# Kernel tuning notes

Hardware: AMD Instinct MI355X
Metric: run time of the kernel (lower is better)

The kernel has to match this reference:

```python
import jax, jax.numpy as jnp
import numpy as np

B, C, H, W = 4, 256, 64, 64
D_STATE, D_CONV, EXPAND = 16, 4, 2
D_INNER = EXPAND * C          # 512
DT_RANK = (C + 15) // 16      # 16 (math.ceil(d_model/16), mamba_ssm default)


def setup_inputs() -> dict:
    key = jax.random.key(0)
    ks = jax.random.split(key, 16)
    s = lambda k, shp, sc=0.02: (jax.random.normal(k, shp, dtype=jnp.float32) * sc)
    inp = {
        "spatial_feat": jax.random.normal(ks[0], (B, C, H, W), dtype=jnp.float32),
        "freq_feat":    jax.random.normal(ks[1], (B, C, H, W), dtype=jnp.float32),
        # fusion proj: Linear(2C -> C)
        "W_proj": s(ks[2], (C, 2 * C)),
        "b_proj": jnp.zeros((C,), jnp.float32),
        # Mamba params (mamba_ssm defaults: bias=False for in/out proj, conv_bias=True)
        "W_in":   s(ks[3], (2 * D_INNER, C)),
        "conv_w": s(ks[4], (D_INNER, 1, D_CONV), 0.1),
        "conv_b": jnp.zeros((D_INNER,), jnp.float32),
        "W_x":    s(ks[5], (DT_RANK + 2 * D_STATE, D_INNER)),
        "W_dt":   s(ks[6], (D_INNER, DT_RANK), 0.1),
        "b_dt":   s(ks[7], (D_INNER,), 0.5),
        "A_log":  jnp.log(jnp.tile(jnp.arange(1, D_STATE + 1, dtype=jnp.float32), (D_INNER, 1))),
        "D":      jnp.ones((D_INNER,), jnp.float32),
        "W_out":  s(ks[8], (C, D_INNER)),
        # LayerNorm
        "ln_gamma": jnp.ones((C,), jnp.float32),
        "ln_beta":  jnp.zeros((C,), jnp.float32),
    }
    return inp


def _mamba(x, W_in, conv_w, conv_b, W_x, W_dt, b_dt, A_log, Dp, W_out):
    # x: [B, L, C]
    Bb, L, _ = x.shape
    xz = jnp.einsum("blc,ec->ble", x, W_in)              # [B,L,2*d_inner]
    u, z = jnp.split(xz, 2, axis=-1)                      # each [B,L,d_inner]
    # causal depthwise conv1d along L
    u_c = jnp.transpose(u, (0, 2, 1))                     # [B,d_inner,L]
    u_c = jax.lax.conv_general_dilated(
        u_c, conv_w, window_strides=(1,), padding=[(D_CONV - 1, 0)],
        dimension_numbers=("NCH", "OIH", "NCH"), feature_group_count=D_INNER)
    u_c = u_c + conv_b[None, :, None]
    u = jax.nn.silu(jnp.transpose(u_c, (0, 2, 1)))        # [B,L,d_inner]
    # input-dependent dt, B, C
    dbc = jnp.einsum("bld,rd->blr", u, W_x)               # [B,L,dt_rank+2*d_state]
    dt = dbc[..., :DT_RANK]
    Bm = dbc[..., DT_RANK:DT_RANK + D_STATE]              # [B,L,d_state]
    Cm = dbc[..., DT_RANK + D_STATE:]                     # [B,L,d_state]
    delta = jax.nn.softplus(jnp.einsum("blr,dr->bld", dt, W_dt) + b_dt)  # [B,L,d_inner]
    A = -jnp.exp(A_log)                                   # [d_inner,d_state]

    def step(h, t):
        delta_t, B_t, C_t, u_t = t                        # [B,di],[B,ds],[B,ds],[B,di]
        dA = jnp.exp(delta_t[..., None] * A)              # [B,di,ds]
        h = h * dA + (delta_t * u_t)[..., None] * B_t[:, None, :]
        y = jnp.einsum("bds,bs->bd", h, C_t)
        return h, y

    tm = lambda a: jnp.swapaxes(a, 0, 1)                  # [B,L,..] -> [L,B,..]
    h0 = jnp.zeros((Bb, D_INNER, D_STATE), x.dtype)
    _, ys = jax.lax.scan(step, h0, (tm(delta), tm(Bm), tm(Cm), tm(u)))
    y = jnp.swapaxes(ys, 0, 1)                            # [B,L,d_inner]
    y = y + u * Dp
    y = y * jax.nn.silu(z)
    return jnp.einsum("bld,cd->blc", y, W_out)            # [B,L,C]


def reference(spatial_feat, freq_feat, W_proj, b_proj, W_in, conv_w, conv_b,
              W_x, W_dt, b_dt, A_log, D, W_out, ln_gamma, ln_beta):
    Bb, Cc, Hh, Ww = spatial_feat.shape
    L = Hh * Ww
    xs = jnp.transpose(spatial_feat.reshape(Bb, Cc, L), (0, 2, 1))  # [B,L,C]
    xf = jnp.transpose(freq_feat.reshape(Bb, Cc, L), (0, 2, 1))
    x_cat = jnp.concatenate([xs, xf], axis=-1)                       # [B,L,2C]
    x_proj = jnp.einsum("ble,ce->blc", x_cat, W_proj) + b_proj       # [B,L,C]
    x_mixed = _mamba(x_proj, W_in, conv_w, conv_b, W_x, W_dt, b_dt, A_log, D, W_out)
    mu = jnp.mean(x_mixed, axis=-1, keepdims=True)
    var = jnp.var(x_mixed, axis=-1, keepdims=True)
    x_out = (x_mixed - mu) * jax.lax.rsqrt(var + 1e-5) * ln_gamma + ln_beta
    return jnp.transpose(x_out, (0, 2, 1)).reshape(Bb, Cc, Hh, Ww)
```

## Files before the change

kernel.cpp:

```cpp
#include <hip/hip_runtime.h>
#include <hip/hip_fp16.h>
#include <math.h>

#define L 4096
#define CDIM 256
#define DIN 512
#define DSTATE 16
#define DTR 16
#define BATCH 4

using f32x4  = __attribute__((ext_vector_type(4))) float;
using f16x8  = __attribute__((ext_vector_type(8))) _Float16;

__device__ __forceinline__ float silu_f(float x) { return x / (1.f + __expf(-x)); }
__device__ __forceinline__ float softplus_fast(float x) {
    return (x > 20.f) ? x : __logf(1.f + __expf(x));
}
__device__ __forceinline__ unsigned pk2h(float a, float b) {
    __half2 h = __floats2half2_rn(a, b);
    return *reinterpret_cast<unsigned*>(&h);
}

#define LDK 40

enum { HEPI_XP = 0, HEPI_UZ = 1, HEPI_F32 = 2, HEPI_D34 = 3 };
template<int EPI, bool A_F32KM, int NT>
__global__ __launch_bounds__(256)
void hgemm(const float* __restrict__ Af0, const float* __restrict__ Af1,
           const __half* __restrict__ Ah_g, const __half* __restrict__ Bh_g,
           const float* __restrict__ bias,
           float* __restrict__ O0, __half* __restrict__ Oh0, __half* __restrict__ Oh1,
           float* __restrict__ Ob, float* __restrict__ Oc,
           int M, int N, int K, int kSplit, long strideAb, int nBlk)
{
    constexpr int BM = 64, MT = 2;
    constexpr int BN = 2 * NT * 16;
    constexpr int BSEG = BN / 64;
    __shared__ __align__(16) _Float16 Ah[2][BM][LDK];
    __shared__ __align__(16) _Float16 Bh[2][BN][LDK];
    const int mBlk = M / BM;
    const int bid = blockIdx.x;
    const int r = bid & 7, q = bid >> 3;
    const int ni = q % nBlk;
    const int mg = (q / nBlk) * 8 + r;
    const int b = mg / mBlk, m_idx = mg - b * mBlk;
    const int n0 = ni * BN, m0 = m_idx * BM;
    const int tid  = threadIdx.x;
    const int lane = tid & 63;
    const int w    = tid >> 6;
    const int wr   = w >> 1, wc = w & 1;
    const int lrow = lane & 15;
    const int loct = lane >> 4;

    f32x4 acc[MT][NT];
    #pragma unroll
    for (int i = 0; i < MT; ++i)
        #pragma unroll
        for (int j = 0; j < NT; ++j)
            acc[i][j] = (f32x4){0.f, 0.f, 0.f, 0.f};

    const int sOct = tid & 3, sRow = tid >> 2;
    float va[8];
    uint4 pa, pb[BSEG];

    auto loadA = [&](int kk) {
        if (A_F32KM) {
            int m = tid & 63, ks = tid >> 6;
            #pragma unroll
            for (int j = 0; j < 8; ++j) {
                int kg = kk + ks * 8 + j;
                const float* Ap; int kl;
                if (kg < kSplit) { Ap = Af0; kl = kg; } else { Ap = Af1; kl = kg - kSplit; }
                va[j] = Ap[(long)b * strideAb + (long)kl * M + m0 + m];
            }
        } else {
            pa = *(const uint4*)(Ah_g + (long)b * strideAb +
                                 (long)(m0 + sRow) * K + kk + sOct * 8);
        }
    };
    auto loadB = [&](int kk) {
        #pragma unroll
        for (int p = 0; p < BSEG; ++p) {
            int ng = n0 + sRow + p * 64;
            if (EPI == HEPI_D34 && ng >= N)
                pb[p] = make_uint4(0, 0, 0, 0);
            else
                pb[p] = *(const uint4*)(Bh_g + (long)ng * K + kk + sOct * 8);
        }
    };
    auto storeAB = [&](int buf) {
        if (A_F32KM) {
            int m = tid & 63, ks = tid >> 6;
            uint4 h;
            h.x = pk2h(va[0], va[1]);
            h.y = pk2h(va[2], va[3]);
            h.z = pk2h(va[4], va[5]);
            h.w = pk2h(va[6], va[7]);
            *(uint4*)&Ah[buf][m][ks * 8] = h;
        } else {
            *(uint4*)&Ah[buf][sRow][sOct * 8] = pa;
        }
        #pragma unroll
        for (int p = 0; p < BSEG; ++p)
            *(uint4*)&Bh[buf][sRow + p * 64][sOct * 8] = pb[p];
    };

    loadA(0); loadB(0);
    storeAB(0);
    __syncthreads();
    int cur = 0;
    for (int kk = 0; kk < K; kk += 32) {
        const bool more = (kk + 32 < K);
        if (more) { loadA(kk + 32); loadB(kk + 32); }
        f16x8 bh[NT];
        #pragma unroll
        for (int nt = 0; nt < NT; ++nt)
            bh[nt] = *(const f16x8*)&Bh[cur][wc*NT*16 + nt*16 + lrow][loct*8];
        #pragma unroll
        for (int mt = 0; mt < MT; ++mt) {
            f16x8 ah = *(const f16x8*)&Ah[cur][wr*MT*16 + mt*16 + lrow][loct*8];
            #pragma unroll
            for (int nt = 0; nt < NT; ++nt)
                acc[mt][nt] = __builtin_amdgcn_mfma_f32_16x16x32_f16(ah, bh[nt], acc[mt][nt], 0, 0, 0);
        }
        if (more) {
            storeAB(cur ^ 1);
            __syncthreads();
            cur ^= 1;
        }
    }
    #pragma unroll
    for (int mt = 0; mt < MT; ++mt) {
        #pragma unroll
        for (int r4 = 0; r4 < 4; ++r4) {
            int m = m0 + wr*MT*16 + mt * 16 + loct * 4 + r4;
            long rowb = (long)b * M + m;
            #pragma unroll
            for (int nt = 0; nt < NT; ++nt) {
                int n = n0 + wc*NT*16 + nt * 16 + lrow;
                float v = acc[mt][nt][r4];
                if (EPI == HEPI_XP) {
                    Oh0[rowb * N + n] = __float2half(v + bias[n]);
                } else if (EPI == HEPI_UZ) {
                    if (n < DIN) Oh0[rowb * DIN + n] = __float2half(v);
                    else         Oh1[rowb * DIN + (n - DIN)] = __float2half(v);
                } else if (EPI == HEPI_D34) {
                    if (n < DTR)           O0[rowb * DTR + n] = v;
                    else if (n < 2 * DTR)  Ob[rowb * 16 + (n - DTR)] = v;
                    else if (n < 48)       Oc[rowb * 16 + (n - 32)] = v;
                } else {
                    O0[rowb * N + n] = v;
                }
            }
        }
    }
}

#define SZ_WP  131072
#define SZ_WIN 262144
#define SZ_WO  131072
#define SZ_WC  24576
__global__ __launch_bounds__(256)
void pack_all(const float* __restrict__ Wp, const float* __restrict__ Win,
              const float* __restrict__ Wout, const float* __restrict__ Wx,
              __half* __restrict__ wph, __half* __restrict__ winh,
              __half* __restrict__ woh, __half* __restrict__ wch)
{
    int i = blockIdx.x * 256 + threadIdx.x;
    if (i < SZ_WP) { wph[i] = __float2half(Wp[i]); return; }
    i -= SZ_WP;
    if (i < SZ_WIN) { winh[i] = __float2half(Win[i]); return; }
    i -= SZ_WIN;
    if (i < SZ_WO) { woh[i] = __float2half(Wout[i]); return; }
    i -= SZ_WO;
    if (i < SZ_WC) wch[i] = __float2half(Wx[i]);
}

__global__ __launch_bounds__(256)
void conv_silu_kernel(const __half* __restrict__ u_pre, const float* __restrict__ cw,
                      const float* __restrict__ cb, __half* __restrict__ u)
{
    long idx = (long)blockIdx.x * blockDim.x + threadIdx.x;
    int d = (int)(idx % DIN);
    long bl = idx / DIN;
    int l = (int)(bl % L);
    long brow = bl - l;
    float v = cb[d];
    #pragma unroll
    for (int j = 0; j < 4; ++j) {
        int li = l - 3 + j;
        if (li >= 0) v += __half2float(u_pre[(brow + li) * DIN + d]) * cw[d * 4 + j];
    }
    u[idx] = __float2half(silu_f(v));
}

#define NC 128
#define LC (L / NC)

__global__ __launch_bounds__(256)
void scan_phase1(const float* __restrict__ dtA, const __half* __restrict__ u,
                 const float* __restrict__ Bm, const float* __restrict__ A_log,
                 const float* __restrict__ Wdt, const float* __restrict__ bdt,
                 float* __restrict__ Asum, float* __restrict__ Xsum)
{
    __shared__ float sB[LC][DSTATE];
    __shared__ float sDt[LC][DTR];
    const int gd = blockIdx.x & 1;
    const int c  = (blockIdx.x >> 1) & (NC - 1);
    const int b  = blockIdx.x >> 8;
    const int d  = gd * 256 + threadIdx.x;
    const int t0 = c * LC;
    float Arow[DSTATE];
    #pragma unroll
    for (int q = 0; q < 4; ++q) {
        float4 v = *(const float4*)&A_log[d * DSTATE + q * 4];
        Arow[q * 4 + 0] = -__expf(v.x);
        Arow[q * 4 + 1] = -__expf(v.y);
        Arow[q * 4 + 2] = -__expf(v.z);
        Arow[q * 4 + 3] = -__expf(v.w);
    }
    float Wrow[DTR];
    #pragma unroll
    for (int q = 0; q < 4; ++q) {
        float4 v = *(const float4*)&Wdt[d * DTR + q * 4];
        Wrow[q * 4 + 0] = v.x; Wrow[q * 4 + 1] = v.y;
        Wrow[q * 4 + 2] = v.z; Wrow[q * 4 + 3] = v.w;
    }
    const float bd = bdt[d];
    for (int i = threadIdx.x; i < LC * DSTATE; i += 256) {
        long row = (long)b * L + t0 + (i >> 4);
        sB[i >> 4][i & 15]  = Bm[row * DSTATE + (i & 15)];
        sDt[i >> 4][i & 15] = dtA[row * DTR + (i & 15)];
    }
    __syncthreads();
    float P[DSTATE], X[DSTATE];
    #pragma unroll
    for (int s = 0; s < DSTATE; ++s) { P[s] = 1.f; X[s] = 0.f; }
    for (int t = 0; t < LC; ++t) {
        long gidx = ((long)b * L + t0 + t) * DIN + d;
        float dp = bd;
        #pragma unroll
        for (int rr = 0; rr < DTR; ++rr) dp += sDt[t][rr] * Wrow[rr];
        float dlt = softplus_fast(dp);
        float du  = dlt * __half2float(u[gidx]);
        #pragma unroll
        for (int s = 0; s < DSTATE; ++s) {
            float a = __expf(dlt * Arow[s]);
            P[s] *= a;
            X[s] = a * X[s] + du * sB[t][s];
        }
    }
    long o = (((long)b * NC + c) * DIN + d) * DSTATE;
    #pragma unroll
    for (int q = 0; q < 4; ++q) {
        *(float4*)&Asum[o + q * 4] = make_float4(P[q*4], P[q*4+1], P[q*4+2], P[q*4+3]);
        *(float4*)&Xsum[o + q * 4] = make_float4(X[q*4], X[q*4+1], X[q*4+2], X[q*4+3]);
    }
}

__global__ __launch_bounds__(256)
void scan_phase2(const float* __restrict__ Asum, float* __restrict__ Xsum)
{
    int lane = blockIdx.x * 256 + threadIdx.x;
    int b = lane / (DIN * DSTATE);
    int rem = lane % (DIN * DSTATE);
    float h = 0.f;
    for (int c = 0; c < NC; ++c) {
        long idx = ((long)b * NC + c) * (DIN * DSTATE) + rem;
        float A = Asum[idx], X = Xsum[idx];
        Xsum[idx] = h;
        h = A * h + X;
    }
}

__global__ __launch_bounds__(256)
void scan_phase3(const float* __restrict__ dtA, const __half* __restrict__ u,
                 const float* __restrict__ Bm, const float* __restrict__ Cm,
                 const __half* __restrict__ z, const float* __restrict__ A_log,
                 const float* __restrict__ Wdt, const float* __restrict__ bdt,
                 const float* __restrict__ Dp, const float* __restrict__ Hinit,
                 __half* __restrict__ y2h)
{
    __shared__ float sB[LC][DSTATE], sC[LC][DSTATE];
    __shared__ float sDt[LC][DTR];
    const int gd = blockIdx.x & 1;
    const int c  = (blockIdx.x >> 1) & (NC - 1);
    const int b  = blockIdx.x >> 8;
    const int d  = gd * 256 + threadIdx.x;
    const int t0 = c * LC;
    float Arow[DSTATE];
    #pragma unroll
    for (int q = 0; q < 4; ++q) {
        float4 v = *(const float4*)&A_log[d * DSTATE + q * 4];
        Arow[q * 4 + 0] = -__expf(v.x);
        Arow[q * 4 + 1] = -__expf(v.y);
        Arow[q * 4 + 2] = -__expf(v.z);
        Arow[q * 4 + 3] = -__expf(v.w);
    }
    float Wrow[DTR];
    #pragma unroll
    for (int q = 0; q < 4; ++q) {
        float4 v = *(const float4*)&Wdt[d * DTR + q * 4];
        Wrow[q * 4 + 0] = v.x; Wrow[q * 4 + 1] = v.y;
        Wrow[q * 4 + 2] = v.z; Wrow[q * 4 + 3] = v.w;
    }
    const float bd = bdt[d];
    for (int i = threadIdx.x; i < LC * DSTATE; i += 256) {
        long row = (long)b * L + t0 + (i >> 4);
        long gidx = row * DSTATE + (i & 15);
        sB[i >> 4][i & 15]  = Bm[gidx];
        sC[i >> 4][i & 15]  = Cm[gidx];
        sDt[i >> 4][i & 15] = dtA[row * DTR + (i & 15)];
    }
    float h[DSTATE];
    {
        long o = (((long)b * NC + c) * DIN + d) * DSTATE;
        #pragma unroll
        for (int q = 0; q < 4; ++q) {
            float4 v = *(const float4*)&Hinit[o + q * 4];
            h[q * 4 + 0] = v.x; h[q * 4 + 1] = v.y;
            h[q * 4 + 2] = v.z; h[q * 4 + 3] = v.w;
        }
    }
    const float Dval = Dp[d];
    __syncthreads();
    for (int t = 0; t < LC; ++t) {
        long gidx = ((long)b * L + t0 + t) * DIN + d;
        float dp = bd;
        #pragma unroll
        for (int rr = 0; rr < DTR; ++rr) dp += sDt[t][rr] * Wrow[rr];
        float dlt = softplus_fast(dp);
        float uu  = __half2float(u[gidx]);
        float zz  = __half2float(z[gidx]);
        float du  = dlt * uu;
        float y = 0.f;
        #pragma unroll
        for (int s = 0; s < DSTATE; ++s) {
            float a = __expf(dlt * Arow[s]);
            h[s] = h[s] * a + du * sB[t][s];
            y += h[s] * sC[t][s];
        }
        y2h[gidx] = __float2half((y + uu * Dval) * silu_f(zz));
    }
}

__global__ __launch_bounds__(256)
void ln_kernel(const float* __restrict__ X, const float* __restrict__ gamma,
               const float* __restrict__ beta, float* __restrict__ out)
{
    __shared__ float tile[32][257];
    __shared__ float sMu[32], sRs[32];
    const int l0 = blockIdx.x * 32;
    const int b  = blockIdx.y;
    const int tid = threadIdx.x;
    for (int i = tid; i < 32 * 256; i += 256) {
        int l = i >> 8, c = i & 255;
        tile[l][c] = X[((long)b * L + l0 + l) * CDIM + c];
    }
    __syncthreads();
    {
        int l = tid >> 3, sub = tid & 7;
        float s1 = 0.f, s2 = 0.f;
        for (int c = sub * 32; c < sub * 32 + 32; ++c) {
            float v = tile[l][c];
            s1 += v; s2 += v * v;
        }
        s1 += __shfl_xor(s1, 1); s2 += __shfl_xor(s2, 1);
        s1 += __shfl_xor(s1, 2); s2 += __shfl_xor(s2, 2);
        s1 += __shfl_xor(s1, 4); s2 += __shfl_xor(s2, 4);
        if (sub == 0) {
            float mu = s1 * (1.f / 256.f);
            float var = s2 * (1.f / 256.f) - mu * mu;
            sMu[l] = mu;
            sRs[l] = rsqrtf(var + 1e-5f);
        }
    }
    __syncthreads();
    for (int i = tid; i < 32 * 256; i += 256) {
        int ll = i & 31, c = i >> 5;
        float v = (tile[ll][c] - sMu[ll]) * sRs[ll] * gamma[c] + beta[c];
        out[((long)b * CDIM + c) * L + l0 + ll] = v;
    }
}

extern "C" void kernel_launch(void* const* d_in, const int* in_sizes, int n_in,
                              void* d_out, int out_size, void* d_ws, size_t ws_size,
                              hipStream_t stream)
{
    const float* sp   = (const float*)d_in[0];
    const float* fq   = (const float*)d_in[1];
    const float* Wp   = (const float*)d_in[2];
    const float* bp   = (const float*)d_in[3];
    const float* Win  = (const float*)d_in[4];
    const float* cw   = (const float*)d_in[5];
    const float* cb   = (const float*)d_in[6];
    const float* Wx   = (const float*)d_in[7];
    const float* Wdt  = (const float*)d_in[8];
    const float* bdt  = (const float*)d_in[9];
    const float* Alog = (const float*)d_in[10];
    const float* Dp   = (const float*)d_in[11];
    const float* Wout = (const float*)d_in[12];
    const float* gam  = (const float*)d_in[13];
    const float* bet  = (const float*)d_in[14];
    float* out = (float*)d_out;
    float* ws  = (float*)d_ws;

    const size_t NLD = (size_t)BATCH * L * DIN;
    const size_t NLC = (size_t)BATCH * L * CDIM;

    size_t off = 0;
    __half* u16   = (__half*)(ws + off); off += NLD / 2;
    __half* u16c  = (__half*)(ws + off); off += NLD / 2;
    __half* z16   = (__half*)(ws + off); off += NLD / 2;
    __half* y16   = (__half*)(ws + off); off += NLD / 2;
    __half* xp16  = (__half*)(ws + off); off += NLC / 2;
    float*  xmix  = ws + off; off += NLC;
    float*  dtA   = ws + off; off += (size_t)BATCH * L * DTR;
    __half* wph   = (__half*)(ws + off); off += SZ_WP / 2;
    __half* winh  = (__half*)(ws + off); off += SZ_WIN / 2;
    __half* woh   = (__half*)(ws + off); off += SZ_WO / 2;
    __half* wch   = (__half*)(ws + off); off += SZ_WC / 2;
    float*  Bmb   = ws + off; off += (size_t)BATCH * L * DSTATE;
    float*  Cmb   = ws + off; off += (size_t)BATCH * L * DSTATE;
    float*  Asum  = ws + off; off += (size_t)BATCH * NC * DIN * DSTATE;
    float*  Xsum  = ws + off; off += (size_t)BATCH * NC * DIN * DSTATE;

    dim3 blk(256);
    pack_all<<<dim3((SZ_WP + SZ_WIN + SZ_WO + SZ_WC) / 256), blk, 0, stream>>>(
        Wp, Win, Wout, Wx, wph, winh, woh, wch);

    hgemm<HEPI_XP, true, 2><<<dim3(BATCH * (L/64) * 4), blk, 0, stream>>>(
        sp, fq, nullptr, wph, bp, nullptr, xp16, nullptr, nullptr, nullptr,
        L, CDIM, 2 * CDIM, CDIM, (long)CDIM * L, 4);
    hgemm<HEPI_UZ, false, 4><<<dim3(BATCH * (L/64) * 8), blk, 0, stream>>>(
        nullptr, nullptr, xp16, winh, nullptr, nullptr, u16, z16, nullptr, nullptr,
        L, 2 * DIN, CDIM, 1 << 30, (long)L * CDIM, 8);
    conv_silu_kernel<<<dim3((int)(NLD / 256)), blk, 0, stream>>>(u16, cw, cb, u16c);
    hgemm<HEPI_D34, false, 2><<<dim3(BATCH * (L/64) * 1), blk, 0, stream>>>(
        nullptr, nullptr, u16c, wch, nullptr, dtA, nullptr, nullptr, Bmb, Cmb,
        L, 48, DIN, 1 << 30, (long)L * DIN, 1);

    scan_phase1<<<dim3(BATCH * NC * 2), blk, 0, stream>>>(
        dtA, u16c, Bmb, Alog, Wdt, bdt, Asum, Xsum);
    scan_phase2<<<dim3(BATCH * DIN * DSTATE / 256), blk, 0, stream>>>(Asum, Xsum);
    scan_phase3<<<dim3(BATCH * NC * 2), blk, 0, stream>>>(
        dtA, u16c, Bmb, Cmb, z16, Alog, Wdt, bdt, Dp, Xsum, y16);

    hgemm<HEPI_F32, false, 2><<<dim3(BATCH * (L/64) * 4), blk, 0, stream>>>(
        nullptr, nullptr, y16, woh, nullptr, xmix, nullptr, nullptr, nullptr, nullptr,
        L, CDIM, DIN, 1 << 30, (long)L * DIN, 4);
    ln_kernel<<<dim3(L / 32, BATCH), blk, 0, stream>>>(xmix, gam, bet, out);
}
```

Before: 344.1 us.

## Stage scan inputs in shared memory, use exp2, interleave chunk summaries, prefetch phase2

The scan phases now preload each chunk's u and z halves into shared memory with vectorized 16-byte loads, and load B, C and dt rows as float4. The per-step exp uses a hardware exp2 builtin with A prescaled by log2(e). Phase 1 writes the chunk decay and state interleaved into one AX buffer, and phase 2 prefetches eight chunks ahead and writes its prefix states to a separate Hout buffer. The dt dot product is split into four partial sums, and phase 3 accumulates y in four partial sums to shorten dependency chains. This aims to cut global-load latency and transcendental cost in the scan, at the price of more shared memory per block and possibly lower occupancy.

```diff
diff --git a/kernel.cpp b/kernel.cpp
--- a/kernel.cpp
+++ b/kernel.cpp
@@ -12,7 +12,17 @@
 using f32x4  = __attribute__((ext_vector_type(4))) float;
 using f16x8  = __attribute__((ext_vector_type(8))) _Float16;
 
-__device__ __forceinline__ float silu_f(float x) { return x / (1.f + __expf(-x)); }
+#define LOG2E 1.44269504088896f
+
+#if __has_builtin(__builtin_amdgcn_exp2f)
+#define EXP2(x) __builtin_amdgcn_exp2f(x)
+#else
+#define EXP2(x) __expf((x) * 0.69314718056f)
+#endif
+
+__device__ __forceinline__ float silu_f(float x) {
+    return __fdividef(x, 1.f + __expf(-x));
+}
 __device__ __forceinline__ float softplus_fast(float x) {
     return (x > 20.f) ? x : __logf(1.f + __expf(x));
 }
@@ -201,75 +211,103 @@
 void scan_phase1(const float* __restrict__ dtA, const __half* __restrict__ u,
                  const float* __restrict__ Bm, const float* __restrict__ A_log,
                  const float* __restrict__ Wdt, const float* __restrict__ bdt,
-                 float* __restrict__ Asum, float* __restrict__ Xsum)
+                 float* __restrict__ AX)
 {
     __shared__ float sB[LC][DSTATE];
     __shared__ float sDt[LC][DTR];
+    __shared__ __half sU[LC][256];
     const int gd = blockIdx.x & 1;
     const int c  = (blockIdx.x >> 1) & (NC - 1);
     const int b  = blockIdx.x >> 8;
-    const int d  = gd * 256 + threadIdx.x;
+    const int tid = threadIdx.x;
+    const int d  = gd * 256 + tid;
     const int t0 = c * LC;
     float Arow[DSTATE];
     #pragma unroll
     for (int q = 0; q < 4; ++q) {
         float4 v = *(const float4*)&A_log[d * DSTATE + q * 4];
-        Arow[q * 4 + 0] = -__expf(v.x);
-        Arow[q * 4 + 1] = -__expf(v.y);
-        Arow[q * 4 + 2] = -__expf(v.z);
-        Arow[q * 4 + 3] = -__expf(v.w);
-    }
-    float Wrow[DTR];
-    #pragma unroll
-    for (int q = 0; q < 4; ++q) {
-        float4 v = *(const float4*)&Wdt[d * DTR + q * 4];
-        Wrow[q * 4 + 0] = v.x; Wrow[q * 4 + 1] = v.y;
-        Wrow[q * 4 + 2] = v.z; Wrow[q * 4 + 3] = v.w;
-    }
+        Arow[q * 4 + 0] = -__expf(v.x) * LOG2E;
+        Arow[q * 4 + 1] = -__expf(v.y) * LOG2E;
+        Arow[q * 4 + 2] = -__expf(v.z) * LOG2E;
+        Arow[q * 4 + 3] = -__expf(v.w) * LOG2E;
+    }
+    const float4 W0 = *(const float4*)&Wdt[d * DTR + 0];
+    const float4 W1 = *(const float4*)&Wdt[d * DTR + 4];
+    const float4 W2 = *(const float4*)&Wdt[d * DTR + 8];
+    const float4 W3 = *(const float4*)&Wdt[d * DTR + 12];
     const float bd = bdt[d];
-    for (int i = threadIdx.x; i < LC * DSTATE; i += 256) {
-        long row = (long)b * L + t0 + (i >> 4);
-        sB[i >> 4][i & 15]  = Bm[row * DSTATE + (i & 15)];
-        sDt[i >> 4][i & 15] = dtA[row * DTR + (i & 15)];
+    {
+        const __half* ub = u + ((long)b * L + t0) * DIN + gd * 256;
+        #pragma unroll
+        for (int j = 0; j < 4; ++j) {
+            int i = tid + j * 256;
+            int t = i >> 5, col = (i & 31) * 8;
+            *(float4*)&sU[t][col] = *(const float4*)&ub[(long)t * DIN + col];
+        }
+        if (tid < 128) {
+            const float* Bb = Bm  + ((long)b * L + t0) * DSTATE;
+            const float* Db = dtA + ((long)b * L + t0) * DTR;
+            *(float4*)&((float*)sB)[tid * 4]  = *(const float4*)&Bb[tid * 4];
+            *(float4*)&((float*)sDt)[tid * 4] = *(const float4*)&Db[tid * 4];
+        }
     }
     __syncthreads();
     float P[DSTATE], X[DSTATE];
     #pragma unroll
     for (int s = 0; s < DSTATE; ++s) { P[s] = 1.f; X[s] = 0.f; }
+    #pragma unroll 2
     for (int t = 0; t < LC; ++t) {
-        long gidx = ((long)b * L + t0 + t) * DIN + d;
-        float dp = bd;
-        #pragma unroll
-        for (int rr = 0; rr < DTR; ++rr) dp += sDt[t][rr] * Wrow[rr];
-        float dlt = softplus_fast(dp);
-        float du  = dlt * __half2float(u[gidx]);
+        float4 q0 = *(const float4*)&sDt[t][0];
+        float4 q1 = *(const float4*)&sDt[t][4];
+        float4 q2 = *(const float4*)&sDt[t][8];
+        float4 q3 = *(const float4*)&sDt[t][12];
+        float dp0 = fmaf(q0.x, W0.x, fmaf(q0.y, W0.y, fmaf(q0.z, W0.z, q0.w * W0.w)));
+        float dp1 = fmaf(q1.x, W1.x, fmaf(q1.y, W1.y, fmaf(q1.z, W1.z, q1.w * W1.w)));
+        float dp2 = fmaf(q2.x, W2.x, fmaf(q2.y, W2.y, fmaf(q2.z, W2.z, q2.w * W2.w)));
+        float dp3 = fmaf(q3.x, W3.x, fmaf(q3.y, W3.y, fmaf(q3.z, W3.z, q3.w * W3.w)));
+        float dlt = softplus_fast(((dp0 + dp1) + (dp2 + dp3)) + bd);
+        float du  = dlt * __half2float(sU[t][tid]);
+        float Brow[DSTATE];
+        *(float4*)&Brow[0]  = *(const float4*)&sB[t][0];
+        *(float4*)&Brow[4]  = *(const float4*)&sB[t][4];
+        *(float4*)&Brow[8]  = *(const float4*)&sB[t][8];
+        *(float4*)&Brow[12] = *(const float4*)&sB[t][12];
         #pragma unroll
         for (int s = 0; s < DSTATE; ++s) {
-            float a = __expf(dlt * Arow[s]);
+            float a = EXP2(dlt * Arow[s]);
             P[s] *= a;
-            X[s] = a * X[s] + du * sB[t][s];
-        }
-    }
-    long o = (((long)b * NC + c) * DIN + d) * DSTATE;
-    #pragma unroll
-    for (int q = 0; q < 4; ++q) {
-        *(float4*)&Asum[o + q * 4] = make_float4(P[q*4], P[q*4+1], P[q*4+2], P[q*4+3]);
-        *(float4*)&Xsum[o + q * 4] = make_float4(X[q*4], X[q*4+1], X[q*4+2], X[q*4+3]);
-    }
-}
-
-__global__ __launch_bounds__(256)
-void scan_phase2(const float* __restrict__ Asum, float* __restrict__ Xsum)
+            X[s] = fmaf(a, X[s], du * Brow[s]);
+        }
+    }
+    long o2 = ((((long)b * NC + c) * DIN + d) * DSTATE) * 2;
+    #pragma unroll
+    for (int q = 0; q < 8; ++q)
+        *(float4*)&AX[o2 + q * 4] =
+            make_float4(P[2*q], X[2*q], P[2*q+1], X[2*q+1]);
+}
+
+__global__ __launch_bounds__(256)
+void scan_phase2(const float* __restrict__ AX, float* __restrict__ Hout)
 {
     int lane = blockIdx.x * 256 + threadIdx.x;
-    int b = lane / (DIN * DSTATE);
-    int rem = lane % (DIN * DSTATE);
+    int b = lane >> 13;
+    int rem = lane & 8191;
+    const long cs = (long)DIN * DSTATE;
+    const long base = (long)b * NC * cs + rem;
     float h = 0.f;
-    for (int c = 0; c < NC; ++c) {
-        long idx = ((long)b * NC + c) * (DIN * DSTATE) + rem;
-        float A = Asum[idx], X = Xsum[idx];
-        Xsum[idx] = h;
-        h = A * h + X;
+    float2 c0, c1, c2, c3, n0, n1, n2, n3;
+    auto ld = [&](int c) -> float2 {
+        return *(const float2*)&AX[2 * (base + (long)c * cs)];
+    };
+    c0 = ld(0); c1 = ld(1); c2 = ld(2); c3 = ld(3);
+    n0 = ld(4); n1 = ld(5); n2 = ld(6); n3 = ld(7);
+    for (int c = 0; c < NC; c += 4) {
+        Hout[base + (long)(c+0) * cs] = h; h = fmaf(c0.x, h, c0.y);
+        Hout[base + (long)(c+1) * cs] = h; h = fmaf(c1.x, h, c1.y);
+        Hout[base + (long)(c+2) * cs] = h; h = fmaf(c2.x, h, c2.y);
+        Hout[base + (long)(c+3) * cs] = h; h = fmaf(c3.x, h, c3.y);
+        c0 = n0; c1 = n1; c2 = n2; c3 = n3;
+        if (c + 8 < NC) { n0 = ld(c+8); n1 = ld(c+9); n2 = ld(c+10); n3 = ld(c+11); }
     }
 }
 
@@ -283,34 +321,46 @@
 {
     __shared__ float sB[LC][DSTATE], sC[LC][DSTATE];
     __shared__ float sDt[LC][DTR];
+    __shared__ __half sU[LC][256];
+    __shared__ __half sZ[LC][256];
     const int gd = blockIdx.x & 1;
     const int c  = (blockIdx.x >> 1) & (NC - 1);
     const int b  = blockIdx.x >> 8;
-    const int d  = gd * 256 + threadIdx.x;
+    const int tid = threadIdx.x;
+    const int d  = gd * 256 + tid;
     const int t0 = c * LC;
     float Arow[DSTATE];
     #pragma unroll
     for (int q = 0; q < 4; ++q) {
         float4 v = *(const float4*)&A_log[d * DSTATE + q * 4];
-        Arow[q * 4 + 0] = -__expf(v.x);
-        Arow[q * 4 + 1] = -__expf(v.y);
-        Arow[q * 4 + 2] = -__expf(v.z);
-        Arow[q * 4 + 3] = -__expf(v.w);
-    }
-    float Wrow[DTR];
-    #pragma unroll
-    for (int q = 0; q < 4; ++q) {
-        float4 v = *(const float4*)&Wdt[d * DTR + q * 4];
-        Wrow[q * 4 + 0] = v.x; Wrow[q * 4 + 1] = v.y;
-        Wrow[q * 4 + 2] = v.z; Wrow[q * 4 + 3] = v.w;
-    }
+        Arow[q * 4 + 0] = -__expf(v.x) * LOG2E;
+        Arow[q * 4 + 1] = -__expf(v.y) * LOG2E;
+        Arow[q * 4 + 2] = -__expf(v.z) * LOG2E;
+        Arow[q * 4 + 3] = -__expf(v.w) * LOG2E;
+    }
+    const float4 W0 = *(const float4*)&Wdt[d * DTR + 0];
+    const float4 W1 = *(const float4*)&Wdt[d * DTR + 4];
+    const float4 W2 = *(const float4*)&Wdt[d * DTR + 8];
+    const float4 W3 = *(const float4*)&Wdt[d * DTR + 12];
     const float bd = bdt[d];
-    for (int i = threadIdx.x; i < LC * DSTATE; i += 256) {
-        long row = (long)b * L + t0 + (i >> 4);
-        long gidx = row * DSTATE + (i & 15);
-        sB[i >> 4][i & 15]  = Bm[gidx];
-        sC[i >> 4][i & 15]  = Cm[gidx];
-        sDt[i >> 4][i & 15] = dtA[row * DTR + (i & 15)];
+    {
+        const __half* ub = u + ((long)b * L + t0) * DIN + gd * 256;
+        const __half* zb = z + ((long)b * L + t0) * DIN + gd * 256;
+        #pragma unroll
+        for (int j = 0; j < 4; ++j) {
+            int i = tid + j * 256;
+            int t = i >> 5, col = (i & 31) * 8;
+            *(float4*)&sU[t][col] = *(const float4*)&ub[(long)t * DIN + col];
+            *(float4*)&sZ[t][col] = *(const float4*)&zb[(long)t * DIN + col];
+        }
+        if (tid < 128) {
+            const float* Bb = Bm  + ((long)b * L + t0) * DSTATE;
+            const float* Cb = Cm  + ((long)b * L + t0) * DSTATE;
+            const float* Db = dtA + ((long)b * L + t0) * DTR;
+            *(float4*)&((float*)sB)[tid * 4]  = *(const float4*)&Bb[tid * 4];
+            *(float4*)&((float*)sC)[tid * 4]  = *(const float4*)&Cb[tid * 4];
+            *(float4*)&((float*)sDt)[tid * 4] = *(const float4*)&Db[tid * 4];
+        }
     }
     float h[DSTATE];
     {
@@ -324,22 +374,47 @@
     }
     const float Dval = Dp[d];
     __syncthreads();
+    #pragma unroll 2
     for (int t = 0; t < LC; ++t) {
+        float4 q0 = *(const float4*)&sDt[t][0];
+        float4 q1 = *(const float4*)&sDt[t][4];
+        float4 q2 = *(const float4*)&sDt[t][8];
+        float4 q3 = *(const float4*)&sDt[t][12];
+        float dp0 = fmaf(q0.x, W0.x, fmaf(q0.y, W0.y, fmaf(q0.z, W0.z, q0.w * W0.w)));
+        float dp1 = fmaf(q1.x, W1.x, fmaf(q1.y, W1.y, fmaf(q1.z, W1.z, q1.w * W1.w)));
+        float dp2 = fmaf(q2.x, W2.x, fmaf(q2.y, W2.y, fmaf(q2.z, W2.z, q2.w * W2.w)));
+        float dp3 = fmaf(q3.x, W3.x, fmaf(q3.y, W3.y, fmaf(q3.z, W3.z, q3.w * W3.w)));
+        float dlt = softplus_fast(((dp0 + dp1) + (dp2 + dp3)) + bd);
+        float uu = __half2float(sU[t][tid]);
+        float zz = __half2float(sZ[t][tid]);
+        float du = dlt * uu;
+        float Brow[DSTATE], Crow[DSTATE];
+        *(float4*)&Brow[0]  = *(const float4*)&sB[t][0];
+        *(float4*)&Brow[4]  = *(const float4*)&sB[t][4];
+        *(float4*)&Brow[8]  = *(const float4*)&sB[t][8];
+        *(float4*)&Brow[12] = *(const float4*)&sB[t][12];
+        *(float4*)&Crow[0]  = *(const float4*)&sC[t][0];
+        *(float4*)&Crow[4]  = *(const float4*)&sC[t][4];
+        *(float4*)&Crow[8]  = *(const float4*)&sC[t][8];
+        *(float4*)&Crow[12] = *(const float4*)&sC[t][12];
+        float y0 = 0.f, y1 = 0.f, y2 = 0.f, y3 = 0.f;
+        #pragma unroll
+        for (int s = 0; s < DSTATE; s += 4) {
+            float a0 = EXP2(dlt * Arow[s+0]);
+            float a1 = EXP2(dlt * Arow[s+1]);
+            float a2 = EXP2(dlt * Arow[s+2]);
+            float a3 = EXP2(dlt * Arow[s+3]);
+            h[s+0] = fmaf(h[s+0], a0, du * Brow[s+0]);
+            h[s+1] = fmaf(h[s+1], a1, du * Brow[s+1]);
+            h[s+2] = fmaf(h[s+2], a2, du * Brow[s+2]);
+            h[s+3] = fmaf(h[s+3], a3, du * Brow[s+3]);
+            y0 = fmaf(h[s+0], Crow[s+0], y0);
+            y1 = fmaf(h[s+1], Crow[s+1], y1);
+            y2 = fmaf(h[s+2], Crow[s+2], y2);
+            y3 = fmaf(h[s+3], Crow[s+3], y3);
+        }
+        float y = (y0 + y1) + (y2 + y3);
         long gidx = ((long)b * L + t0 + t) * DIN + d;
-        float dp = bd;
-        #pragma unroll
-        for (int rr = 0; rr < DTR; ++rr) dp += sDt[t][rr] * Wrow[rr];
-        float dlt = softplus_fast(dp);
-        float uu  = __half2float(u[gidx]);
-        float zz  = __half2float(z[gidx]);
-        float du  = dlt * uu;
-        float y = 0.f;
-        #pragma unroll
-        for (int s = 0; s < DSTATE; ++s) {
-            float a = __expf(dlt * Arow[s]);
-            h[s] = h[s] * a + du * sB[t][s];
-            y += h[s] * sC[t][s];
-        }
         y2h[gidx] = __float2half((y + uu * Dval) * silu_f(zz));
     }
 }
@@ -422,8 +497,8 @@
     __half* wch   = (__half*)(ws + off); off += SZ_WC / 2;
     float*  Bmb   = ws + off; off += (size_t)BATCH * L * DSTATE;
     float*  Cmb   = ws + off; off += (size_t)BATCH * L * DSTATE;
-    float*  Asum  = ws + off; off += (size_t)BATCH * NC * DIN * DSTATE;
-    float*  Xsum  = ws + off; off += (size_t)BATCH * NC * DIN * DSTATE;
+    float*  AX    = ws + off; off += (size_t)BATCH * NC * DIN * DSTATE * 2;
+    float*  Hout  = ws + off; off += (size_t)BATCH * NC * DIN * DSTATE;
 
     dim3 blk(256);
     pack_all<<<dim3((SZ_WP + SZ_WIN + SZ_WO + SZ_WC) / 256), blk, 0, stream>>>(
@@ -441,10 +516,10 @@
         L, 48, DIN, 1 << 30, (long)L * DIN, 1);
 
     scan_phase1<<<dim3(BATCH * NC * 2), blk, 0, stream>>>(
-        dtA, u16c, Bmb, Alog, Wdt, bdt, Asum, Xsum);
-    scan_phase2<<<dim3(BATCH * DIN * DSTATE / 256), blk, 0, stream>>>(Asum, Xsum);
+        dtA, u16c, Bmb, Alog, Wdt, bdt, AX);
+    scan_phase2<<<dim3(BATCH * DIN * DSTATE / 256), blk, 0, stream>>>(AX, Hout);
     scan_phase3<<<dim3(BATCH * NC * 2), blk, 0, stream>>>(
-        dtA, u16c, Bmb, Cmb, z16, Alog, Wdt, bdt, Dp, Xsum, y16);
+        dtA, u16c, Bmb, Cmb, z16, Alog, Wdt, bdt, Dp, Hout, y16);
 
     hgemm<HEPI_F32, false, 2><<<dim3(BATCH * (L/64) * 4), blk, 0, stream>>>(
         nullptr, nullptr, y16, woh, nullptr, xmix, nullptr, nullptr, nullptr, nullptr,
```

New measurement: 333.8 us. 1.03x faster.
